# Kernel tuning notes

Measured on AMD Instinct MI355X. Metric: run time of the kernel, lower is better.

Reference implementation:

```python
import jax, jax.numpy as jnp
import numpy as np

THRESHOLD_IOU = 0.8  # forward default in the original module


def setup_inputs() -> dict:
    key = jax.random.key(0)
    k1, k2, k3, k4 = jax.random.split(key, 4)
    N = M = 16
    H = W = 768
    # Binary masks (the original zeroes pixels to 0.0 and tests >0 via torch.where)
    masks_a = (jax.random.uniform(k1, (N, H, W)) > 0.6).astype(jnp.float32)
    masks_b = (jax.random.uniform(k2, (M, H, W)) > 0.6).astype(jnp.float32)
    # Make a few masks identical across labels so the IoU>threshold (suppression)
    # branch is exercised, not just the partial-overlap zeroing branch.
    masks_b = masks_b.at[:4].set(masks_a[:4])
    scores_a = jax.random.uniform(k3, (N,))
    scores_b = jax.random.uniform(k4, (M,))
    return {"masks_a": masks_a, "masks_b": masks_b,
            "scores_a": scores_a, "scores_b": scores_b}


def _overlap_filter(masks_a, masks_b, scores_a, scores_b, thr):
    # Sequential pairwise IoU + overlap zeroing, faithful to the original
    # nested product(enumerate(masks), enumerate(other_masks)) loop order
    # (i outer, j inner), where each pair sees masks already modified by
    # earlier pairs. Pruning ("keep") is applied after the loop; here it is
    # represented with static shapes as keep flags + zeroed-out rows.
    N, H, W = masks_a.shape
    M = masks_b.shape[0]
    P = H * W
    A0 = masks_a.reshape(N, P)
    B0 = masks_b.reshape(M, P)

    def body(carry, k):
        A, B, fi, fj = carry
        i = k // M
        j = k % M
        a = A[i]  # [P]
        b = B[j]  # [P]
        abin = a > 0
        bbin = b > 0
        inter = abin & bbin
        inter_sum = jnp.sum(inter.astype(jnp.float32))
        union_sum = jnp.sum((abin | bbin).astype(jnp.float32))
        iou = inter_sum / jnp.maximum(union_sum, 1.0)
        a_wins = scores_a[i] > scores_b[j]
        suppress = iou > thr                 # mark whole loser mask for removal
        zero_case = (iou > 0) & ~suppress    # zero overlapped pixels of loser
        b_new = jnp.where(zero_case & a_wins & inter, 0.0, b)
        a_new = jnp.where(zero_case & (~a_wins) & inter, 0.0, a)
        A = A.at[i].set(a_new)
        B = B.at[j].set(b_new)
        fj = fj.at[j].set(fj[j] | (suppress & a_wins))
        fi = fi.at[i].set(fi[i] | (suppress & ~a_wins))
        return (A, B, fi, fj), None

    fi0 = jnp.zeros(N, dtype=bool)
    fj0 = jnp.zeros(M, dtype=bool)
    (A, B, fi, fj), _ = jax.lax.scan(body, (A0, B0, fi0, fj0), jnp.arange(N * M))
    keep_a = ~fi
    keep_b = ~fj
    A = jnp.where(keep_a[:, None], A, 0.0)
    B = jnp.where(keep_b[:, None], B, 0.0)
    return A.reshape(N, H, W), B.reshape(M, H, W), keep_a, keep_b


def reference(masks_a, masks_b, scores_a, scores_b):
    return _overlap_filter(masks_a, masks_b, scores_a, scores_b, THRESHOLD_IOU)
```

## Files before the change

kernel.cpp:

```cpp
#include <hip/hip_runtime.h>
#include <stdint.h>

#define NM 16
#define HW_P 589824
#define U8PM 9216
#define C4PM 4608
#define F4PM 147456
#define F4PT 2359296
#define PT 512
#define NG 8
#define EWG 64

typedef unsigned long long u64;
typedef float vf4 __attribute__((ext_vector_type(4)));


__device__ __forceinline__ unsigned aload(const unsigned* p) {
    return __hip_atomic_load(p, __ATOMIC_RELAXED, __HIP_MEMORY_SCOPE_AGENT);
}
__device__ __forceinline__ void astore(unsigned* p, unsigned v) {
    __hip_atomic_store(p, v, __ATOMIC_RELAXED, __HIP_MEMORY_SCOPE_AGENT);
}
__device__ __forceinline__ unsigned afadd(unsigned* p, unsigned v) {
    return __hip_atomic_fetch_add(p, v, __ATOMIC_RELAXED, __HIP_MEMORY_SCOPE_AGENT);
}

__device__ __forceinline__ uint32_t spread4(uint32_t x) {
    uint32_t t = (x | (x << 12)) & 0x000F000Fu;
    t = (t | (t << 6)) & 0x03030303u;
    t = (t | (t << 3)) & 0x11111111u;
    return t;
}

__global__ __launch_bounds__(256) void binarize_kernel(
    const float* __restrict__ ma, const float* __restrict__ mb,
    uint32_t* __restrict__ bitsA, uint32_t* __restrict__ bitsB,
    uint4* __restrict__ meta4)
{
    if (blockIdx.x == 0) {
        uint4 z; z.x = z.y = z.z = z.w = 0u;
        meta4[threadIdx.x] = z;
        meta4[threadIdx.x + 256] = z;
    }
    int g = blockIdx.x * 256 + threadIdx.x;
    int tensor = (g >= F4PT);
    int lg = tensor ? (g - F4PT) : g;
    const float* src = tensor ? mb : ma;
    vf4 v = __builtin_nontemporal_load(((const vf4*)src) + lg);
    u64 q0 = __ballot(v.x > 0.0f);
    u64 q1 = __ballot(v.y > 0.0f);
    u64 q2 = __ballot(v.z > 0.0f);
    u64 q3 = __ballot(v.w > 0.0f);
    int lane = threadIdx.x & 63;
    if (lane < 8) {
        uint32_t wd = spread4((uint32_t)(q0 >> (8 * lane)) & 0xFFu)
                    | (spread4((uint32_t)(q1 >> (8 * lane)) & 0xFFu) << 1)
                    | (spread4((uint32_t)(q2 >> (8 * lane)) & 0xFFu) << 2)
                    | (spread4((uint32_t)(q3 >> (8 * lane)) & 0xFFu) << 3);
        uint32_t* bits = tensor ? bitsB : bitsA;
        bits[((lg & ~63) >> 3) + lane] = wd;
    }
}

__global__ __launch_bounds__(PT, 1) void pipeline_kernel(
    const float* __restrict__ sa, const float* __restrict__ sb,
    uint32_t* bitsA, uint32_t* bitsB, unsigned* meta, u64* msg)
{
    unsigned* cnt    = meta;
    unsigned* winner = meta + 8;
    int* flagsA      = (int*)(meta + 16);
    int* flagsB      = (int*)(meta + 32);
    unsigned* prodF  = meta + 80;

    const int tid = threadIdx.x;
    const int wave = tid >> 6, lane = tid & 63;

    __shared__ int s_g;
    __shared__ int4 part[8];

    if (tid == 0) {
        int xcc;
        asm volatile("s_getreg_b32 %0, hwreg(HW_REG_XCC_ID)" : "=s"(xcc));
        xcc &= 7;
        unsigned slot = afadd(&cnt[xcc], 1u);
        int mine = -1;
        if (slot < NG) {
            if (slot == NG - 1) {
                unsigned exp = 0u;
                __hip_atomic_compare_exchange_strong(
                    winner, &exp, (unsigned)(xcc + 1),
                    __ATOMIC_RELAXED, __ATOMIC_RELAXED, __HIP_MEMORY_SCOPE_AGENT);
            }
            unsigned w;
            while (!(w = aload(winner))) __builtin_amdgcn_s_sleep(1);
            if (w == (unsigned)(xcc + 1)) mine = (int)slot;
        }
        s_g = mine;
    }
    __syncthreads();
    const int g = s_g;
    if (g < 0) return;

    const int c0 = 2 * g, c1 = 2 * g + 1;
    uint4* A4 = (uint4*)bitsA;
    uint4* B4 = (uint4*)bitsB;

    u64 b0[18], b1[18];

    int v0 = 0, v1 = 0;
#pragma unroll
    for (int w = 0; w < 9; ++w) {
        uint4 q0 = B4[(size_t)c0 * C4PM + tid + PT * w];
        uint4 q1 = B4[(size_t)c1 * C4PM + tid + PT * w];
        b0[2 * w] = ((u64)q0.y << 32) | q0.x; b0[2 * w + 1] = ((u64)q0.w << 32) | q0.z;
        b1[2 * w] = ((u64)q1.y << 32) | q1.x; b1[2 * w + 1] = ((u64)q1.w << 32) | q1.z;
        v0 += __popcll(b0[2 * w]) + __popcll(b0[2 * w + 1]);
        v1 += __popcll(b1[2 * w]) + __popcll(b1[2 * w + 1]);
    }
#pragma unroll
    for (int off = 32; off >= 1; off >>= 1) {
        v0 += __shfl_xor(v0, off); v1 += __shfl_xor(v1, off);
    }
    if (lane == 0) { int4 p; p.x = v0; p.y = v1; p.z = 0; p.w = 0; part[wave] = p; }
    __syncthreads();
    int pcb0 = 0, pcb1 = 0;
#pragma unroll
    for (int w = 0; w < 8; ++w) { pcb0 += part[w].x; pcb1 += part[w].y; }
    float sb0 = sb[c0], sb1 = sb[c1];
    int fb0 = 0, fb1 = 0;
    __syncthreads();

    for (int t = 0; t < NM; ++t) {
        int pca, fa;
        u64 a[18];

        if (g == 0) {
            pca = 0; fa = 0;
#pragma unroll
            for (int w = 0; w < 9; ++w) {
                uint4 q = A4[(size_t)t * C4PM + tid + PT * w];
                a[2 * w] = ((u64)q.y << 32) | q.x;
                a[2 * w + 1] = ((u64)q.w << 32) | q.z;
            }
        } else {
            const unsigned* fptr = &prodF[((g - 1) * 16 + t) * 4];
            unsigned v;
            do { v = aload(fptr); } while (!v);
            asm volatile("" ::: "memory");
            pca = (int)((v >> 1) & 0xFFFFFu);
            fa  = (int)((v >> 21) & 1u);
            const uint4* s4 = (const uint4*)(msg + (size_t)((g - 1) * 16 + t) * U8PM);
#pragma unroll
            for (int w = 0; w < 9; ++w) {
                uint4 q = s4[tid + PT * w];
                a[2 * w]     = ((u64)q.y << 32) | q.x;
                a[2 * w + 1] = ((u64)q.w << 32) | q.z;
            }
        }

        int i0 = 0, i1 = 0, itr = 0, ipc = 0;
#pragma unroll
        for (int w = 0; w < 18; ++w) {
            u64 ab0 = a[w] & b0[w];
            i0 += __popcll(ab0);
            i1 += __popcll(a[w] & b1[w]);
            itr += __popcll(ab0 & b1[w]);
        }
        if (g == 0) {
#pragma unroll
            for (int w = 0; w < 18; ++w) ipc += __popcll(a[w]);
        }
#pragma unroll
        for (int off = 32; off >= 1; off >>= 1) {
            i0 += __shfl_xor(i0, off); i1 += __shfl_xor(i1, off);
            itr += __shfl_xor(itr, off); ipc += __shfl_xor(ipc, off);
        }
        if (lane == 0) {
            int4 p; p.x = i0; p.y = i1; p.z = itr; p.w = ipc; part[wave] = p;
        }
        __syncthreads();
        int I0 = 0, I1 = 0, T = 0, PC = 0;
#pragma unroll
        for (int w = 0; w < 8; ++w) {
            int4 p = part[w];
            I0 += p.x; I1 += p.y; T += p.z; PC += p.w;
        }
        if (g == 0) pca = PC;

        float sai = sa[t];
        bool aupd = false;
        {
            int inter = I0;
            int uni = pca + pcb0 - inter;
            float iou = (float)inter / fmaxf((float)uni, 1.0f);
            bool aw = sai > sb0;
            if (iou > 0.8f) { if (aw) fb0 = 1; else fa = 1; }
            else if (inter > 0) {
                if (aw) {
                    pcb0 -= inter;
#pragma unroll
                    for (int w = 0; w < 18; ++w) b0[w] &= ~a[w];
                } else {
                    pca -= inter; aupd = true;
#pragma unroll
                    for (int w = 0; w < 18; ++w) a[w] &= ~b0[w];
                }
            }
        }
        {
            int inter = aupd ? (I1 - T) : I1;
            int uni = pca + pcb1 - inter;
            float iou = (float)inter / fmaxf((float)uni, 1.0f);
            bool aw = sai > sb1;
            if (iou > 0.8f) { if (aw) fb1 = 1; else fa = 1; }
            else if (inter > 0) {
                if (aw) {
                    pcb1 -= inter;
#pragma unroll
                    for (int w = 0; w < 18; ++w) b1[w] &= ~a[w];
                } else {
                    pca -= inter;
#pragma unroll
                    for (int w = 0; w < 18; ++w) a[w] &= ~b1[w];
                }
            }
        }

        if (g < NG - 1) {
            uint4* so = (uint4*)(msg + (size_t)(g * 16 + t) * U8PM);
#pragma unroll
            for (int w = 0; w < 9; ++w) {
                uint4 q;
                q.x = (uint32_t)a[2 * w];     q.y = (uint32_t)(a[2 * w] >> 32);
                q.z = (uint32_t)a[2 * w + 1]; q.w = (uint32_t)(a[2 * w + 1] >> 32);
                so[tid + PT * w] = q;
            }
            __syncthreads();
            if (tid == 0)
                astore(&prodF[(g * 16 + t) * 4],
                       1u | ((unsigned)pca << 1) | ((unsigned)fa << 21));
        } else {
            uint4* Ar = A4 + (size_t)t * C4PM;
#pragma unroll
            for (int w = 0; w < 9; ++w) {
                uint4 q;
                q.x = (uint32_t)a[2 * w];     q.y = (uint32_t)(a[2 * w] >> 32);
                q.z = (uint32_t)a[2 * w + 1]; q.w = (uint32_t)(a[2 * w + 1] >> 32);
                Ar[tid + PT * w] = q;
            }
            if (tid == 0) flagsA[t] = fa;
            __syncthreads();
        }
    }

    uint4* Wc0 = B4 + (size_t)c0 * C4PM;
    uint4* Wc1 = B4 + (size_t)c1 * C4PM;
#pragma unroll
    for (int w = 0; w < 9; ++w) {
        uint4 q0, q1;
        q0.x = (uint32_t)b0[2 * w];     q0.y = (uint32_t)(b0[2 * w] >> 32);
        q0.z = (uint32_t)b0[2 * w + 1]; q0.w = (uint32_t)(b0[2 * w + 1] >> 32);
        q1.x = (uint32_t)b1[2 * w];     q1.y = (uint32_t)(b1[2 * w] >> 32);
        q1.z = (uint32_t)b1[2 * w + 1]; q1.w = (uint32_t)(b1[2 * w + 1] >> 32);
        Wc0[tid + PT * w] = q0;
        Wc1[tid + PT * w] = q1;
    }
    if (tid == 0) { flagsB[c0] = fb0; flagsB[c1] = fb1; }
}

__global__ __launch_bounds__(256) void expand_kernel(
    const uint32_t* __restrict__ bitsA, const uint32_t* __restrict__ bitsB,
    const int* __restrict__ meta, float* __restrict__ out)
{
    int g = blockIdx.x * 256 + threadIdx.x;
    int tensor = (g >= F4PT);
    int lg = tensor ? (g - F4PT) : g;
    const uint32_t* bits = tensor ? bitsB : bitsA;
    const int* flags = meta + (tensor ? 32 : 16);
    int m = lg / F4PM;
    bool keep = (flags[m] == 0);
    uint32_t wd = keep ? bits[lg >> 3] : 0u;
    int sh = (lg & 7) * 4;
    vf4 o;
    o.x = ((wd >> (sh + 0)) & 1u) ? 1.0f : 0.0f;
    o.y = ((wd >> (sh + 1)) & 1u) ? 1.0f : 0.0f;
    o.z = ((wd >> (sh + 2)) & 1u) ? 1.0f : 0.0f;
    o.w = ((wd >> (sh + 3)) & 1u) ? 1.0f : 0.0f;
    __builtin_nontemporal_store(o, ((vf4*)out) + g);
    if (g < 2 * NM) {
        out[(size_t)2 * NM * HW_P + g] = meta[16 + g] ? 0.0f : 1.0f;
    }
}

extern "C" void kernel_launch(void* const* d_in, const int* in_sizes, int n_in,
                              void* d_out, int out_size, void* d_ws, size_t ws_size,
                              hipStream_t stream)
{
    const float* ma = (const float*)d_in[0];
    const float* mb = (const float*)d_in[1];
    const float* sa = (const float*)d_in[2];
    const float* sb = (const float*)d_in[3];
    float* out = (float*)d_out;
    char* ws = (char*)d_ws;

    uint32_t* bitsA = (uint32_t*)(ws);
    uint32_t* bitsB = (uint32_t*)(ws + 1179648);
    unsigned* meta  = (unsigned*)(ws + 2359296);
    u64* msg        = (u64*)(ws + 2367488);

    binarize_kernel<<<18432, 256, 0, stream>>>(ma, mb, bitsA, bitsB,
                                               (uint4*)meta);
    pipeline_kernel<<<EWG, PT, 0, stream>>>(sa, sb, bitsA, bitsB, meta, msg);
    expand_kernel<<<18432, 256, 0, stream>>>(bitsA, bitsB, (const int*)meta, out);
}
```

Measured before the change: 220.5 us.

## Process two A masks per pipeline step with precomputed inclusion-exclusion counts

Each pipeline stage now handles two rows of A per step instead of one. That halves the number of inter-block handoffs, spin-waits, block barriers and reductions. The intersection counts for all four pairs are computed in one pass, using extra triple and quadruple AND popcounts, so the sequential IoU updates can be resolved through inclusion-exclusion. The cost is more registers (another 18 u64 array), doubled message size, and a more complex correctness argument for the count adjustments.

```diff
diff --git a/kernel.cpp b/kernel.cpp
--- a/kernel.cpp
+++ b/kernel.cpp
@@ -9,6 +9,7 @@
 #define F4PT 2359296
 #define PT 512
 #define NG 8
+#define NT 8
 #define EWG 64
 
 typedef unsigned long long u64;
@@ -18,7 +19,10 @@
 __device__ __forceinline__ unsigned aload(const unsigned* p) {
     return __hip_atomic_load(p, __ATOMIC_RELAXED, __HIP_MEMORY_SCOPE_AGENT);
 }
-__device__ __forceinline__ void astore(unsigned* p, unsigned v) {
+__device__ __forceinline__ u64 aload64(const u64* p) {
+    return __hip_atomic_load(p, __ATOMIC_RELAXED, __HIP_MEMORY_SCOPE_AGENT);
+}
+__device__ __forceinline__ void astore64(u64* p, u64 v) {
     __hip_atomic_store(p, v, __ATOMIC_RELAXED, __HIP_MEMORY_SCOPE_AGENT);
 }
 __device__ __forceinline__ unsigned afadd(unsigned* p, unsigned v) {
@@ -70,13 +74,13 @@
     unsigned* winner = meta + 8;
     int* flagsA      = (int*)(meta + 16);
     int* flagsB      = (int*)(meta + 32);
-    unsigned* prodF  = meta + 80;
+    u64* prodF       = (u64*)(meta + 80);
 
     const int tid = threadIdx.x;
     const int wave = tid >> 6, lane = tid & 63;
 
     __shared__ int s_g;
-    __shared__ int4 part[8];
+    __shared__ int part[8][12];
 
     if (tid == 0) {
         int xcc;
@@ -107,164 +111,205 @@
 
     u64 b0[18], b1[18];
 
+    auto load18 = [&](const uint4* s4, u64* d) {
+#pragma unroll
+        for (int w = 0; w < 9; ++w) {
+            uint4 q = s4[tid + PT * w];
+            d[2 * w]     = ((u64)q.y << 32) | q.x;
+            d[2 * w + 1] = ((u64)q.w << 32) | q.z;
+        }
+    };
+    auto store18 = [&](uint4* s4, const u64* d) {
+#pragma unroll
+        for (int w = 0; w < 9; ++w) {
+            uint4 q;
+            q.x = (uint32_t)d[2 * w];     q.y = (uint32_t)(d[2 * w] >> 32);
+            q.z = (uint32_t)d[2 * w + 1]; q.w = (uint32_t)(d[2 * w + 1] >> 32);
+            s4[tid + PT * w] = q;
+        }
+    };
+
+    load18(B4 + (size_t)c0 * C4PM, b0);
+    load18(B4 + (size_t)c1 * C4PM, b1);
     int v0 = 0, v1 = 0;
 #pragma unroll
-    for (int w = 0; w < 9; ++w) {
-        uint4 q0 = B4[(size_t)c0 * C4PM + tid + PT * w];
-        uint4 q1 = B4[(size_t)c1 * C4PM + tid + PT * w];
-        b0[2 * w] = ((u64)q0.y << 32) | q0.x; b0[2 * w + 1] = ((u64)q0.w << 32) | q0.z;
-        b1[2 * w] = ((u64)q1.y << 32) | q1.x; b1[2 * w + 1] = ((u64)q1.w << 32) | q1.z;
-        v0 += __popcll(b0[2 * w]) + __popcll(b0[2 * w + 1]);
-        v1 += __popcll(b1[2 * w]) + __popcll(b1[2 * w + 1]);
-    }
+    for (int w = 0; w < 18; ++w) { v0 += __popcll(b0[w]); v1 += __popcll(b1[w]); }
 #pragma unroll
     for (int off = 32; off >= 1; off >>= 1) {
         v0 += __shfl_xor(v0, off); v1 += __shfl_xor(v1, off);
     }
-    if (lane == 0) { int4 p; p.x = v0; p.y = v1; p.z = 0; p.w = 0; part[wave] = p; }
+    if (lane == 0) { part[wave][0] = v0; part[wave][1] = v1; }
     __syncthreads();
     int pcb0 = 0, pcb1 = 0;
 #pragma unroll
-    for (int w = 0; w < 8; ++w) { pcb0 += part[w].x; pcb1 += part[w].y; }
+    for (int w = 0; w < 8; ++w) { pcb0 += part[w][0]; pcb1 += part[w][1]; }
     float sb0 = sb[c0], sb1 = sb[c1];
     int fb0 = 0, fb1 = 0;
     __syncthreads();
 
-    for (int t = 0; t < NM; ++t) {
-        int pca, fa;
-        u64 a[18];
+    for (int rt = 0; rt < NT; ++rt) {
+        const int i0 = 2 * rt, i1 = i0 + 1;
+        int pca0, pca1, fa0, fa1;
+        u64 a0[18], a1[18];
 
         if (g == 0) {
-            pca = 0; fa = 0;
-#pragma unroll
-            for (int w = 0; w < 9; ++w) {
-                uint4 q = A4[(size_t)t * C4PM + tid + PT * w];
-                a[2 * w] = ((u64)q.y << 32) | q.x;
-                a[2 * w + 1] = ((u64)q.w << 32) | q.z;
-            }
+            load18(A4 + (size_t)i0 * C4PM, a0);
+            load18(A4 + (size_t)i1 * C4PM, a1);
+            pca0 = pca1 = 0; fa0 = fa1 = 0;
         } else {
-            const unsigned* fptr = &prodF[((g - 1) * 16 + t) * 4];
-            unsigned v;
-            do { v = aload(fptr); } while (!v);
+            const u64* fptr = &prodF[(g - 1) * 8 + rt];
+            u64 v;
+            do { v = aload64(fptr); } while (!(v >> 63));
             asm volatile("" ::: "memory");
-            pca = (int)((v >> 1) & 0xFFFFFu);
-            fa  = (int)((v >> 21) & 1u);
-            const uint4* s4 = (const uint4*)(msg + (size_t)((g - 1) * 16 + t) * U8PM);
-#pragma unroll
-            for (int w = 0; w < 9; ++w) {
-                uint4 q = s4[tid + PT * w];
-                a[2 * w]     = ((u64)q.y << 32) | q.x;
-                a[2 * w + 1] = ((u64)q.w << 32) | q.z;
-            }
-        }
-
-        int i0 = 0, i1 = 0, itr = 0, ipc = 0;
-#pragma unroll
-        for (int w = 0; w < 18; ++w) {
-            u64 ab0 = a[w] & b0[w];
-            i0 += __popcll(ab0);
-            i1 += __popcll(a[w] & b1[w]);
-            itr += __popcll(ab0 & b1[w]);
-        }
-        if (g == 0) {
-#pragma unroll
-            for (int w = 0; w < 18; ++w) ipc += __popcll(a[w]);
-        }
-#pragma unroll
-        for (int off = 32; off >= 1; off >>= 1) {
-            i0 += __shfl_xor(i0, off); i1 += __shfl_xor(i1, off);
-            itr += __shfl_xor(itr, off); ipc += __shfl_xor(ipc, off);
-        }
+            pca0 = (int)(v & 0xFFFFF);
+            pca1 = (int)((v >> 20) & 0xFFFFF);
+            fa0  = (int)((v >> 40) & 1u);
+            fa1  = (int)((v >> 41) & 1u);
+            const uint4* s4 = (const uint4*)(msg + (size_t)((g - 1) * 8 + rt) * 18432);
+            load18(s4, a0);
+            load18(s4 + C4PM, a1);
+        }
+
+        int tt[11];
+        {
+            int s0=0,s1=0,s2=0,s3=0,s4_=0,s5=0,s6=0,s7=0,s8=0,p0=0,p1=0;
+#pragma unroll
+            for (int w = 0; w < 18; ++w) {
+                u64 A0 = a0[w], A1 = a1[w], B0 = b0[w], B1 = b1[w];
+                u64 ab  = A0 & B0;
+                u64 ab1 = A0 & B1;
+                u64 cb  = A1 & B0;
+                u64 cb1 = A1 & B1;
+                s0 += __popcll(ab);
+                s1 += __popcll(ab1);
+                s2 += __popcll(ab & B1);
+                s3 += __popcll(cb);
+                s4_ += __popcll(cb & A0);
+                s5 += __popcll(cb1);
+                s6 += __popcll(cb1 & A0);
+                s7 += __popcll(cb1 & B0);
+                s8 += __popcll(cb1 & B0 & A0);
+            }
+            if (g == 0) {
+#pragma unroll
+                for (int w = 0; w < 18; ++w) { p0 += __popcll(a0[w]); p1 += __popcll(a1[w]); }
+            }
+            tt[0]=s0; tt[1]=s1; tt[2]=s2; tt[3]=s3; tt[4]=s4_;
+            tt[5]=s5; tt[6]=s6; tt[7]=s7; tt[8]=s8; tt[9]=p0; tt[10]=p1;
+        }
+#pragma unroll
+        for (int off = 32; off >= 1; off >>= 1)
+#pragma unroll
+            for (int i = 0; i < 11; ++i) tt[i] += __shfl_xor(tt[i], off);
         if (lane == 0) {
-            int4 p; p.x = i0; p.y = i1; p.z = itr; p.w = ipc; part[wave] = p;
+#pragma unroll
+            for (int i = 0; i < 11; ++i) part[wave][i] = tt[i];
         }
         __syncthreads();
-        int I0 = 0, I1 = 0, T = 0, PC = 0;
-#pragma unroll
-        for (int w = 0; w < 8; ++w) {
-            int4 p = part[w];
-            I0 += p.x; I1 += p.y; T += p.z; PC += p.w;
-        }
-        if (g == 0) pca = PC;
-
-        float sai = sa[t];
-        bool aupd = false;
-        {
-            int inter = I0;
-            int uni = pca + pcb0 - inter;
+        int T[9], PC0 = 0, PC1 = 0;
+        {
+            int acc[11];
+#pragma unroll
+            for (int i = 0; i < 11; ++i) acc[i] = 0;
+#pragma unroll
+            for (int w = 0; w < 8; ++w)
+#pragma unroll
+                for (int i = 0; i < 11; ++i) acc[i] += part[w][i];
+#pragma unroll
+            for (int i = 0; i < 9; ++i) T[i] = acc[i];
+            PC0 = acc[9]; PC1 = acc[10];
+        }
+        if (g == 0) { pca0 = PC0; pca1 = PC1; }
+
+        float sa0 = sa[i0], sa1 = sa[i1];
+        bool a0l = false, b0l = false, b1l = false, a1l = false;
+        {
+            int inter = T[0];
+            int uni = pca0 + pcb0 - inter;
             float iou = (float)inter / fmaxf((float)uni, 1.0f);
-            bool aw = sai > sb0;
-            if (iou > 0.8f) { if (aw) fb0 = 1; else fa = 1; }
+            bool aw = sa0 > sb0;
+            if (iou > 0.8f) { if (aw) fb0 = 1; else fa0 = 1; }
             else if (inter > 0) {
-                if (aw) {
-                    pcb0 -= inter;
-#pragma unroll
-                    for (int w = 0; w < 18; ++w) b0[w] &= ~a[w];
-                } else {
-                    pca -= inter; aupd = true;
-#pragma unroll
-                    for (int w = 0; w < 18; ++w) a[w] &= ~b0[w];
-                }
-            }
-        }
-        {
-            int inter = aupd ? (I1 - T) : I1;
-            int uni = pca + pcb1 - inter;
+                if (aw) { pcb0 -= inter; b0l = true;
+#pragma unroll
+                          for (int w = 0; w < 18; ++w) b0[w] &= ~a0[w]; }
+                else    { pca0 -= inter; a0l = true;
+#pragma unroll
+                          for (int w = 0; w < 18; ++w) a0[w] &= ~b0[w]; }
+            }
+        }
+        {
+            int inter = T[1] - (a0l ? T[2] : 0);
+            int uni = pca0 + pcb1 - inter;
             float iou = (float)inter / fmaxf((float)uni, 1.0f);
-            bool aw = sai > sb1;
-            if (iou > 0.8f) { if (aw) fb1 = 1; else fa = 1; }
+            bool aw = sa0 > sb1;
+            if (iou > 0.8f) { if (aw) fb1 = 1; else fa0 = 1; }
             else if (inter > 0) {
-                if (aw) {
-                    pcb1 -= inter;
-#pragma unroll
-                    for (int w = 0; w < 18; ++w) b1[w] &= ~a[w];
-                } else {
-                    pca -= inter;
-#pragma unroll
-                    for (int w = 0; w < 18; ++w) a[w] &= ~b1[w];
-                }
+                if (aw) { pcb1 -= inter; b1l = true;
+#pragma unroll
+                          for (int w = 0; w < 18; ++w) b1[w] &= ~a0[w]; }
+                else    { pca0 -= inter;
+#pragma unroll
+                          for (int w = 0; w < 18; ++w) a0[w] &= ~b1[w]; }
+            }
+        }
+        {
+            int inter = T[3] - (b0l ? T[4] : 0);
+            int uni = pca1 + pcb0 - inter;
+            float iou = (float)inter / fmaxf((float)uni, 1.0f);
+            bool aw = sa1 > sb0;
+            if (iou > 0.8f) { if (aw) fb0 = 1; else fa1 = 1; }
+            else if (inter > 0) {
+                if (aw) { pcb0 -= inter;
+#pragma unroll
+                          for (int w = 0; w < 18; ++w) b0[w] &= ~a1[w]; }
+                else    { pca1 -= inter; a1l = true;
+#pragma unroll
+                          for (int w = 0; w < 18; ++w) a1[w] &= ~b0[w]; }
+            }
+        }
+        {
+            int termA = T[5] - (b1l ? (T[6] - (a0l ? T[8] : 0)) : 0);
+            int inter = termA;
+            if (a1l) {
+                int termB = (T[7] - (b0l ? T[8] : 0))
+                          - ((b1l && !a0l && !b0l) ? T[8] : 0);
+                inter = termA - termB;
+            }
+            int uni = pca1 + pcb1 - inter;
+            float iou = (float)inter / fmaxf((float)uni, 1.0f);
+            bool aw = sa1 > sb1;
+            if (iou > 0.8f) { if (aw) fb1 = 1; else fa1 = 1; }
+            else if (inter > 0) {
+                if (aw) { pcb1 -= inter;
+#pragma unroll
+                          for (int w = 0; w < 18; ++w) b1[w] &= ~a1[w]; }
+                else    { pca1 -= inter;
+#pragma unroll
+                          for (int w = 0; w < 18; ++w) a1[w] &= ~b1[w]; }
             }
         }
 
         if (g < NG - 1) {
-            uint4* so = (uint4*)(msg + (size_t)(g * 16 + t) * U8PM);
-#pragma unroll
-            for (int w = 0; w < 9; ++w) {
-                uint4 q;
-                q.x = (uint32_t)a[2 * w];     q.y = (uint32_t)(a[2 * w] >> 32);
-                q.z = (uint32_t)a[2 * w + 1]; q.w = (uint32_t)(a[2 * w + 1] >> 32);
-                so[tid + PT * w] = q;
-            }
+            uint4* so = (uint4*)(msg + (size_t)(g * 8 + rt) * 18432);
+            store18(so, a0);
+            store18(so + C4PM, a1);
             __syncthreads();
             if (tid == 0)
-                astore(&prodF[(g * 16 + t) * 4],
-                       1u | ((unsigned)pca << 1) | ((unsigned)fa << 21));
+                astore64(&prodF[g * 8 + rt],
+                         (1ull << 63) | (u64)(unsigned)pca0
+                         | ((u64)(unsigned)pca1 << 20)
+                         | ((u64)(unsigned)fa0 << 40) | ((u64)(unsigned)fa1 << 41));
         } else {
-            uint4* Ar = A4 + (size_t)t * C4PM;
-#pragma unroll
-            for (int w = 0; w < 9; ++w) {
-                uint4 q;
-                q.x = (uint32_t)a[2 * w];     q.y = (uint32_t)(a[2 * w] >> 32);
-                q.z = (uint32_t)a[2 * w + 1]; q.w = (uint32_t)(a[2 * w + 1] >> 32);
-                Ar[tid + PT * w] = q;
-            }
-            if (tid == 0) flagsA[t] = fa;
+            store18(A4 + (size_t)i0 * C4PM, a0);
+            store18(A4 + (size_t)i1 * C4PM, a1);
+            if (tid == 0) { flagsA[i0] = fa0; flagsA[i1] = fa1; }
             __syncthreads();
         }
     }
 
-    uint4* Wc0 = B4 + (size_t)c0 * C4PM;
-    uint4* Wc1 = B4 + (size_t)c1 * C4PM;
-#pragma unroll
-    for (int w = 0; w < 9; ++w) {
-        uint4 q0, q1;
-        q0.x = (uint32_t)b0[2 * w];     q0.y = (uint32_t)(b0[2 * w] >> 32);
-        q0.z = (uint32_t)b0[2 * w + 1]; q0.w = (uint32_t)(b0[2 * w + 1] >> 32);
-        q1.x = (uint32_t)b1[2 * w];     q1.y = (uint32_t)(b1[2 * w] >> 32);
-        q1.z = (uint32_t)b1[2 * w + 1]; q1.w = (uint32_t)(b1[2 * w + 1] >> 32);
-        Wc0[tid + PT * w] = q0;
-        Wc1[tid + PT * w] = q1;
-    }
+    store18(B4 + (size_t)c0 * C4PM, b0);
+    store18(B4 + (size_t)c1 * C4PM, b1);
     if (tid == 0) { flagsB[c0] = fb0; flagsB[c1] = fb1; }
 }
 
```

After: 387.2 us. 75.6% more time.
